# Kernel optimization log

Measured on AMD Instinct MI355X. Metric: run time of the kernel, lower is better.

Reference implementation:

```python
import jax, jax.numpy as jnp
import numpy as np

NUM_HEADS = 2
LN_EPS = 1e-5


def layer_norm(x, w, b):
    mu = jnp.mean(x, axis=-1, keepdims=True)
    var = jnp.mean(jnp.square(x - mu), axis=-1, keepdims=True)
    return (x - mu) * jax.lax.rsqrt(var + LN_EPS) * w + b


def setup_inputs() -> dict:
    key = jax.random.key(0)
    ks = jax.random.split(key, 8)
    B, N, C = 8, 2048, 1024
    H = 2 * C  # mlp hidden
    s = lambda fan_in: 1.0 / np.sqrt(fan_in)
    return {
        "x": jax.random.normal(ks[0], (B, N, C), dtype=jnp.float32),
        "ln1_w": jnp.ones((C,), jnp.float32),
        "ln1_b": jnp.zeros((C,), jnp.float32),
        "qkv_w": jax.random.normal(ks[1], (C, 3 * C), jnp.float32) * s(C),
        "qkv_b": jnp.zeros((3 * C,), jnp.float32),
        "proj_w": jax.random.normal(ks[2], (C, C), jnp.float32) * s(C),
        "proj_b": jnp.zeros((C,), jnp.float32),
        "ln2_w": jnp.ones((C,), jnp.float32),
        "ln2_b": jnp.zeros((C,), jnp.float32),
        "mlp_w1": jax.random.normal(ks[3], (C, H), jnp.float32) * s(C),
        "mlp_b1": jnp.zeros((H,), jnp.float32),
        "mlp_w2": jax.random.normal(ks[4], (H, C), jnp.float32) * s(H),
        "mlp_b2": jnp.zeros((C,), jnp.float32),
    }


def reference(x, ln1_w, ln1_b, qkv_w, qkv_b, proj_w, proj_b, ln2_w, ln2_b,
              mlp_w1, mlp_b1, mlp_w2, mlp_b2):
    B, N, C = x.shape
    h = NUM_HEADS
    d = C // h
    scale = d ** -0.5

    # --- attention branch ---
    xn = layer_norm(x, ln1_w, ln1_b)
    qkv = (xn @ qkv_w + qkv_b).reshape(B, N, 3, h, d)
    q, k, v = jnp.moveaxis(qkv, 2, 0)          # each [B, N, h, d]
    q = jnp.swapaxes(q, 1, 2)                  # [B, h, N, d]
    k = jnp.swapaxes(k, 1, 2)
    v = jnp.swapaxes(v, 1, 2)
    attn = jnp.einsum("bhnd,bhmd->bhnm", q, k) * scale
    attn = jax.nn.softmax(attn, axis=-1)       # [B, h, N, N]
    out = jnp.einsum("bhnm,bhmd->bhnd", attn, v)
    out = jnp.swapaxes(out, 1, 2).reshape(B, N, C)
    out = out @ proj_w + proj_b
    x = x + out

    # --- mlp branch ---
    xn = layer_norm(x, ln2_w, ln2_b)
    hdn = jax.nn.gelu(xn @ mlp_w1 + mlp_b1, approximate=False)
    x = x + (hdn @ mlp_w2 + mlp_b2)
    return x
```

## Files before the change

kernel.cpp:

```cpp
#include <hip/hip_runtime.h>
#include <hip/hip_bf16.h>
#include <math.h>

#define TILE 128
#define BK 32

using short8  = __attribute__((ext_vector_type(8))) short;
using short4v = __attribute__((ext_vector_type(4))) short;
using f32x4   = __attribute__((ext_vector_type(4))) float;
typedef __hip_bfloat16 bf16;

constexpr int BB = 8, SEQ = 2048, C = 1024, H3 = 3072, DH = 512, MH = 2048;
constexpr int MR = BB * SEQ;

enum {
  F_TRANSB = 1,
  F_GELU   = 2,
  F_RES    = 4,
  F_OUTBF16= 8,
  F_BIAS   = 16,
  F_SCALE  = 32,
  F_RESF32 = 64
};

struct ZOffs { long long a[16]; long long b[16]; long long c[16]; };

__device__ __forceinline__ float bf2f(bf16 h) { return __bfloat162float(h); }

__device__ __forceinline__ void gload16(const void* g, void* l) {
  __builtin_amdgcn_global_load_lds(
      (const __attribute__((address_space(1))) unsigned int*)g,
      (__attribute__((address_space(3))) unsigned int*)l, 16, 0, 0);
}

template<int FLAGS>
__global__ __launch_bounds__(256) void gemm_k(
    const bf16* __restrict__ A,
    const bf16* __restrict__ B,
    void* __restrict__ Dst,
    const float* __restrict__ bias,
    const void* __restrict__ res,
    int K, int lda, int ldb, int ldc,
    float scale, ZOffs zo)
{
  __shared__ __align__(16) unsigned short As[TILE * BK];
  __shared__ __align__(16) unsigned short Bs[TILE * BK];
  const int tid = threadIdx.x;
  const int z = blockIdx.z;
  const int m0 = blockIdx.y * TILE, n0 = blockIdx.x * TILE;
  const bf16* Ab = A + zo.a[z];
  const bf16* Bb = B + zo.b[z];
  const long long coff = zo.c[z];
  const int wave = tid >> 6, lane = tid & 63;
  const int wm = (wave & 1) << 6, wn = (wave >> 1) << 6;
  const int lr = lane & 15, lq = lane >> 4;

  int srow[2], skb[2];
  #pragma unroll
  for (int i = 0; i < 2; i++) {
    int c = tid + (i << 8);
    srow[i] = c >> 2;
    skb[i]  = (c & 3) ^ ((srow[i] >> 1) & 3);
  }
  const bf16* Asrc[2]; const bf16* Bsrc[2] = {nullptr, nullptr};
  #pragma unroll
  for (int i = 0; i < 2; i++)
    Asrc[i] = Ab + (size_t)(m0 + srow[i]) * lda + skb[i] * 8;
  if (FLAGS & F_TRANSB) {
    #pragma unroll
    for (int i = 0; i < 2; i++)
      Bsrc[i] = Bb + (size_t)(n0 + srow[i]) * ldb + skb[i] * 8;
  }

  f32x4 acc[4][4] = {};
  const int swl = (lr >> 1) & 3;

  for (int k0 = 0; k0 < K; k0 += BK) {
    #pragma unroll
    for (int i = 0; i < 2; i++)
      gload16(Asrc[i] + k0, &As[(tid + (i << 8)) * 8]);
    if (FLAGS & F_TRANSB) {
      #pragma unroll
      for (int i = 0; i < 2; i++)
        gload16(Bsrc[i] + k0, &Bs[(tid + (i << 8)) * 8]);
    } else {
      #pragma unroll
      for (int i = 0; i < 2; i++) {
        int c = tid + (i << 8);
        int kk = c >> 4, nn = (c & 15) << 3;
        unsigned short tmp[8];
        *(uint4*)tmp = *(const uint4*)(Bb + (size_t)(k0 + kk) * ldb + n0 + nn);
        #pragma unroll
        for (int j = 0; j < 8; j++) {
          int n = nn + j;
          Bs[n * BK + (((kk >> 3) ^ ((n >> 1) & 3)) << 3) + (kk & 7)] = tmp[j];
        }
      }
    }
    __syncthreads();
    short8 af[4], bfr[4];
    #pragma unroll
    for (int mi = 0; mi < 4; mi++)
      af[mi] = *(const short8*)&As[(wm + mi * 16 + lr) * BK + ((lq ^ swl) << 3)];
    #pragma unroll
    for (int ni = 0; ni < 4; ni++)
      bfr[ni] = *(const short8*)&Bs[(wn + ni * 16 + lr) * BK + ((lq ^ swl) << 3)];
    #pragma unroll
    for (int mi = 0; mi < 4; mi++)
      #pragma unroll
      for (int ni = 0; ni < 4; ni++)
        acc[mi][ni] = __builtin_amdgcn_mfma_f32_16x16x32_bf16(
            af[mi], bfr[ni], acc[mi][ni], 0, 0, 0);
    __syncthreads();
  }

  #pragma unroll
  for (int mi = 0; mi < 4; mi++) {
    #pragma unroll
    for (int ni = 0; ni < 4; ni++) {
      int col = n0 + wn + ni * 16 + lr;
      float bv = (FLAGS & F_BIAS) ? bias[col] : 0.0f;
      #pragma unroll
      for (int r = 0; r < 4; r++) {
        int row = m0 + wm + mi * 16 + lq * 4 + r;
        float v = acc[mi][ni][r];
        if (FLAGS & F_SCALE) v *= scale;
        v += bv;
        if (FLAGS & F_GELU) v = 0.5f * v * (1.0f + erff(v * 0.70710678118654752f));
        if (FLAGS & F_RES) {
          size_t ridx = (size_t)row * ldc + col;
          v += (FLAGS & F_RESF32) ? ((const float*)res)[ridx]
                                  : bf2f(((const bf16*)res)[ridx]);
        }
        size_t idx = (size_t)coff + (size_t)row * ldc + col;
        if (FLAGS & F_OUTBF16) ((bf16*)Dst)[idx] = __float2bfloat16(v);
        else                   ((float*)Dst)[idx] = v;
      }
    }
  }
}

template<int FLAGS>
__global__ __launch_bounds__(512, 2) void gemm256_k(
    const bf16* __restrict__ A,
    const bf16* __restrict__ B,
    void* __restrict__ Dst,
    const float* __restrict__ bias,
    const void* __restrict__ res,
    int K, int lda, int ldb, int ldc,
    float scale, ZOffs zo)
{
  static_assert(FLAGS & F_TRANSB, "gemm256_k requires B^T layout");
  extern __shared__ __align__(16) unsigned short smem[];

  const int tid = threadIdx.x;
  const int z = blockIdx.z;

  const int gx = gridDim.x;
  const int nwg = gx * gridDim.y;
  const int wg = blockIdx.y * gx + blockIdx.x;
  const int cpx = nwg >> 3;
  const int swz = (wg & 7) * cpx + (wg >> 3);
  const int m0 = (swz / gx) * 256, n0 = (swz % gx) * 256;

  const bf16* Ab = A + zo.a[z];
  const bf16* Bb = B + zo.b[z];
  const long long coff = zo.c[z];
  const int wave = tid >> 6, lane = tid & 63;
  const int wm = wave >> 2, wn = wave & 3;
  const int lr = lane & 15, lq = lane >> 4;
  const int swl = (lr >> 1) & 3;
  const int kcol = (lq ^ swl) << 3;

  const int c0 = tid, c1 = tid + 512;
  const int row0 = c0 >> 2, sl0 = (c0 & 3) ^ ((row0 >> 1) & 3);
  const int row1 = c1 >> 2, sl1 = (c1 & 3) ^ ((row1 >> 1) & 3);
  const bf16* sA0 = Ab + (size_t)(m0 + row0) * lda + sl0 * 8;
  const bf16* sA1 = Ab + (size_t)(m0 + row1) * lda + sl1 * 8;
  const bf16* sB0 = Bb + (size_t)(n0 + row0) * ldb + sl0 * 8;
  const bf16* sB1 = Bb + (size_t)(n0 + row1) * ldb + sl1 * 8;
  const int dst0 = c0 * 8, dst1 = c1 * 8;

  const int nt = K >> 5;

#define STAGE(ks_, D_)                                                         \
  do {                                                                         \
    gload16(sA0 + (ks_), (D_) + dst0);                                         \
    gload16(sA1 + (ks_), (D_) + dst1);                                         \
    gload16(sB0 + (ks_), (D_) + 8192 + dst0);                                  \
    gload16(sB1 + (ks_), (D_) + 8192 + dst1);                                  \
  } while (0)

  STAGE(0, smem);
  if (nt > 1) STAGE(32, smem + 16384);

  f32x4 acc[8][4] = {};
  short8 af[4], bf4[4];
  int bc = 0, bs = 2;

  for (int t = 0; t < nt; ++t) {
    if (t == nt - 1) asm volatile("s_waitcnt vmcnt(0)" ::: "memory");
    else             asm volatile("s_waitcnt vmcnt(4)" ::: "memory");
    __builtin_amdgcn_s_barrier();
    asm volatile("" ::: "memory");

    if (t + 2 < nt) STAGE((t + 2) * 32, smem + bs * 16384);

    const unsigned short* At = smem + bc * 16384;
    const unsigned short* Bt = At + 8192;

    #pragma unroll
    for (int n_ = 0; n_ < 4; ++n_)
      bf4[n_] = *(const short8*)&Bt[(wn * 64 + n_ * 16 + lr) * 32 + kcol];
    #pragma unroll
    for (int mh = 0; mh < 2; ++mh) {
      #pragma unroll
      for (int m_ = 0; m_ < 4; ++m_)
        af[m_] = *(const short8*)&At[(wm * 128 + mh * 64 + m_ * 16 + lr) * 32 + kcol];
      __builtin_amdgcn_s_setprio(1);
      #pragma unroll
      for (int m_ = 0; m_ < 4; ++m_)
        #pragma unroll
        for (int n_ = 0; n_ < 4; ++n_)
          acc[mh * 4 + m_][n_] = __builtin_amdgcn_mfma_f32_16x16x32_bf16(
              af[m_], bf4[n_], acc[mh * 4 + m_][n_], 0, 0, 0);
      __builtin_amdgcn_s_setprio(0);
    }
    bc = bc == 2 ? 0 : bc + 1;
    bs = bs == 2 ? 0 : bs + 1;
  }

#undef STAGE

  const int colBase = n0 + wn * 64 + lr;
  float bv[4];
  #pragma unroll
  for (int n = 0; n < 4; ++n)
    bv[n] = (FLAGS & F_BIAS) ? bias[colBase + n * 16] : 0.0f;
  #pragma unroll
  for (int m = 0; m < 8; ++m) {
    #pragma unroll
    for (int n = 0; n < 4; ++n) {
      const int col = colBase + n * 16;
      #pragma unroll
      for (int r = 0; r < 4; ++r) {
        const int row = m0 + wm * 128 + m * 16 + lq * 4 + r;
        float v = acc[m][n][r];
        if (FLAGS & F_SCALE) v *= scale;
        v += bv[n];
        if (FLAGS & F_GELU) v = 0.5f * v * (1.0f + erff(v * 0.70710678118654752f));
        if (FLAGS & F_RES) {
          size_t ridx = (size_t)row * ldc + col;
          v += (FLAGS & F_RESF32) ? ((const float*)res)[ridx]
                                  : bf2f(((const bf16*)res)[ridx]);
        }
        size_t idx = (size_t)coff + (size_t)row * ldc + col;
        if (FLAGS & F_OUTBF16) ((bf16*)Dst)[idx] = __float2bfloat16(v);
        else                   ((float*)Dst)[idx] = v;
      }
    }
  }
}

__global__ __launch_bounds__(256) void tconv_kernel(
    const float* __restrict__ src, bf16* __restrict__ dst, int K, int N)
{
  __shared__ float t[32][33];
  int n0 = blockIdx.x * 32, k0 = blockIdx.y * 32;
  int c = threadIdx.x & 31, r = threadIdx.x >> 5;
  #pragma unroll
  for (int i = 0; i < 4; i++)
    t[r + i * 8][c] = src[(size_t)(k0 + r + i * 8) * N + n0 + c];
  __syncthreads();
  #pragma unroll
  for (int i = 0; i < 4; i++)
    dst[(size_t)(n0 + r + i * 8) * K + k0 + c] = __float2bfloat16(t[c][r + i * 8]);
}

__global__ __launch_bounds__(256) void vtrans_kernel(
    const bf16* __restrict__ qkv, bf16* __restrict__ vt)
{
  __shared__ unsigned short t[32][33];
  int bh = blockIdx.z, b = bh >> 1, h = bh & 1;
  int n0 = blockIdx.x * 32, d0 = blockIdx.y * 32;
  int c = threadIdx.x & 31, r = threadIdx.x >> 5;
  const bf16* src = qkv + (size_t)b * SEQ * H3 + 2 * C + (size_t)h * DH;
  #pragma unroll
  for (int i = 0; i < 4; i++)
    t[r + i * 8][c] = *(const unsigned short*)&src[(size_t)(n0 + r + i * 8) * H3 + d0 + c];
  __syncthreads();
  bf16* dst = vt + ((size_t)bh * DH + d0) * SEQ + n0;
  #pragma unroll
  for (int i = 0; i < 4; i++)
    *(unsigned short*)&dst[(size_t)(r + i * 8) * SEQ + c] = t[c][r + i * 8];
}

__device__ __forceinline__ void ld4(const float* p, float v[4]) {
  const float4 t = *(const float4*)p;
  v[0] = t.x; v[1] = t.y; v[2] = t.z; v[3] = t.w;
}
__device__ __forceinline__ void ld4(const bf16* p, float v[4]) {
  short4v t = *(const short4v*)p;
  #pragma unroll
  for (int i = 0; i < 4; ++i) v[i] = bf2f(((const bf16*)&t)[i]);
}

template<typename T>
__global__ __launch_bounds__(256) void ln_kernel(
    const T* __restrict__ x,
    const float* __restrict__ w,
    const float* __restrict__ b,
    bf16* __restrict__ out)
{
  __shared__ float sm[4], sm2[4];
  int row = blockIdx.x, tid = threadIdx.x;
  float v[4];
  ld4(x + (size_t)row * 1024 + tid * 4, v);
  float s  = v[0] + v[1] + v[2] + v[3];
  float sq = v[0]*v[0] + v[1]*v[1] + v[2]*v[2] + v[3]*v[3];
  #pragma unroll
  for (int o = 32; o > 0; o >>= 1) {
    s  += __shfl_down(s, o, 64);
    sq += __shfl_down(sq, o, 64);
  }
  int wvi = tid >> 6, lnn = tid & 63;
  if (lnn == 0) { sm[wvi] = s; sm2[wvi] = sq; }
  __syncthreads();
  s  = sm[0] + sm[1] + sm[2] + sm[3];
  sq = sm2[0] + sm2[1] + sm2[2] + sm2[3];
  float mean = s * (1.0f / 1024.0f);
  float var  = sq * (1.0f / 1024.0f) - mean * mean;
  float rs = rsqrtf(var + 1e-5f);
  float wv4[4], bv4[4];
  ld4(w + tid * 4, wv4);
  ld4(b + tid * 4, bv4);
  short4v o4;
  #pragma unroll
  for (int i = 0; i < 4; ++i)
    ((bf16*)&o4)[i] = __float2bfloat16((v[i] - mean) * rs * wv4[i] + bv4[i]);
  *(short4v*)&out[(size_t)row * 1024 + tid * 4] = o4;
}

__global__ __launch_bounds__(256) void softmax_kernel(
    bf16* __restrict__ sc)
{
  __shared__ float sm[4];
  int tid = threadIdx.x;
  size_t base = ((size_t)blockIdx.y * 2048 + blockIdx.x) * 2048 + (size_t)tid * 8;
  short8 sv = *(const short8*)&sc[base];
  float v[8], m = -1e30f;
  #pragma unroll
  for (int i = 0; i < 8; i++) { v[i] = bf2f(((const bf16*)&sv)[i]); m = fmaxf(m, v[i]); }
  #pragma unroll
  for (int o = 32; o > 0; o >>= 1) m = fmaxf(m, __shfl_down(m, o, 64));
  int wvi = tid >> 6, lnn = tid & 63;
  if (lnn == 0) sm[wvi] = m;
  __syncthreads();
  m = fmaxf(fmaxf(sm[0], sm[1]), fmaxf(sm[2], sm[3]));
  __syncthreads();
  float s = 0.f;
  #pragma unroll
  for (int i = 0; i < 8; i++) { v[i] = __expf(v[i] - m); s += v[i]; }
  #pragma unroll
  for (int o = 32; o > 0; o >>= 1) s += __shfl_down(s, o, 64);
  if (lnn == 0) sm[wvi] = s;
  __syncthreads();
  s = sm[0] + sm[1] + sm[2] + sm[3];
  float inv = 1.0f / s;
  short8 ov;
  #pragma unroll
  for (int i = 0; i < 8; i++)
    ((bf16*)&ov)[i] = __float2bfloat16(v[i] * inv);
  *(short8*)&sc[base] = ov;
}

#define G256(FL, grid_, A_, B_, D_, bias_, res_, K_, lda_, ldb_, ldc_, sc_, zo_)      \
  do {                                                                                \
    (void)hipFuncSetAttribute(reinterpret_cast<const void*>(&gemm256_k<(FL)>),        \
                              hipFuncAttributeMaxDynamicSharedMemorySize, 98304);     \
    hipLaunchKernelGGL((gemm256_k<(FL)>), grid_, dim3(512), 98304, stream,            \
                       A_, B_, D_, bias_, res_, K_, lda_, ldb_, ldc_, sc_, zo_);      \
  } while (0)

extern "C" void kernel_launch(void* const* d_in, const int* in_sizes, int n_in,
                              void* d_out, int out_size, void* d_ws, size_t ws_size,
                              hipStream_t stream) {
  const float* x      = (const float*)d_in[0];
  const float* ln1_w  = (const float*)d_in[1];
  const float* ln1_b  = (const float*)d_in[2];
  const float* qkv_w  = (const float*)d_in[3];
  const float* qkv_b  = (const float*)d_in[4];
  const float* proj_w = (const float*)d_in[5];
  const float* proj_b = (const float*)d_in[6];
  const float* ln2_w  = (const float*)d_in[7];
  const float* ln2_b  = (const float*)d_in[8];
  const float* mlp_w1 = (const float*)d_in[9];
  const float* mlp_b1 = (const float*)d_in[10];
  const float* mlp_w2 = (const float*)d_in[11];
  const float* mlp_b2 = (const float*)d_in[12];
  float* out = (float*)d_out;

  char* ws = (char*)d_ws;
  const size_t MB = 1ull << 20;
  bf16* qkvT  = (bf16*)ws;
  bf16* projT = qkvT + 3 * 1024 * 1024;
  bf16* w1T   = qkvT + 4 * 1024 * 1024;
  bf16* w2T   = qkvT + 6 * 1024 * 1024;
  bf16* xn    = (bf16*)(ws + 16 * MB);
  bf16* qkvb  = (bf16*)(ws + 48 * MB);
  bf16* h1    = qkvb;
  bf16* Vt    = (bf16*)(ws + 144 * MB);

  int CH; bool useVt, x1f32;
  if      (ws_size >= 304 * MB) { CH = 16; useVt = true;  x1f32 = true;  }
  else if (ws_size >= 240 * MB) { CH = 8;  useVt = true;  x1f32 = true;  }
  else if (ws_size >= 208 * MB) { CH = 4;  useVt = true;  x1f32 = false; }
  else                          { CH = 4;  useVt = false; x1f32 = false; }
  char* R = ws + (useVt ? 176 * MB : 144 * MB);
  bf16*  scores = (bf16*)R;
  float* x1f    = (float*)R;
  bf16*  x1h    = (bf16*)R;

  ZOffs z0 = {};
  const float scale = 0.04419417382415922f;
  dim3 blk(256);

  hipLaunchKernelGGL(tconv_kernel, dim3(H3 / 32, C / 32), blk, 0, stream, qkv_w, qkvT, C, H3);
  hipLaunchKernelGGL(tconv_kernel, dim3(C / 32, C / 32), blk, 0, stream, proj_w, projT, C, C);
  hipLaunchKernelGGL(tconv_kernel, dim3(MH / 32, C / 32), blk, 0, stream, mlp_w1, w1T, C, MH);
  hipLaunchKernelGGL(tconv_kernel, dim3(C / 32, MH / 32), blk, 0, stream, mlp_w2, w2T, MH, C);

  hipLaunchKernelGGL((ln_kernel<float>), dim3(MR), blk, 0, stream, x, ln1_w, ln1_b, xn);

  G256(F_TRANSB | F_BIAS | F_OUTBF16, dim3(H3 / 256, MR / 256, 1),
       xn, qkvT, (void*)qkvb, qkv_b, nullptr, C, C, C, H3, 1.0f, z0);

  if (useVt)
    hipLaunchKernelGGL(vtrans_kernel, dim3(SEQ / 32, DH / 32, 16), blk, 0, stream, qkvb, Vt);

  for (int ch = 0; ch < 16 / CH; ch++) {
    ZOffs zq = {}, zp = {};
    for (int zz = 0; zz < CH; zz++) {
      int bh = ch * CH + zz, b = bh >> 1, hh = bh & 1;
      zq.a[zz] = (long long)b * SEQ * H3 + (long long)hh * DH;
      zq.b[zz] = (long long)b * SEQ * H3 + C + (long long)hh * DH;
      zq.c[zz] = (long long)zz * SEQ * SEQ;
      zp.a[zz] = (long long)zz * SEQ * SEQ;
      zp.b[zz] = useVt ? (long long)bh * DH * SEQ
                       : (long long)b * SEQ * H3 + 2 * C + (long long)hh * DH;
      zp.c[zz] = (long long)b * SEQ * C + (long long)hh * DH;
    }
    G256(F_TRANSB | F_SCALE | F_OUTBF16, dim3(SEQ / 256, SEQ / 256, CH),
         qkvb, qkvb, (void*)scores, nullptr, nullptr, DH, H3, H3, SEQ, scale, zq);
    hipLaunchKernelGGL(softmax_kernel, dim3(SEQ, CH), blk, 0, stream, scores);
    if (useVt)
      G256(F_TRANSB | F_OUTBF16, dim3(DH / 256, SEQ / 256, CH),
           scores, Vt, (void*)xn, nullptr, nullptr, SEQ, SEQ, SEQ, C, 1.0f, zp);
    else
      hipLaunchKernelGGL((gemm_k<F_OUTBF16>),
                         dim3(DH / TILE, SEQ / TILE, CH), blk, 0, stream,
                         scores, qkvb, (void*)xn, nullptr, nullptr, SEQ, SEQ, H3, C, 1.0f, zp);
  }

  if (x1f32) {
    G256(F_TRANSB | F_BIAS | F_RES | F_RESF32, dim3(C / 256, MR / 256, 1),
         xn, projT, (void*)x1f, proj_b, (const void*)x, C, C, C, C, 1.0f, z0);
    hipLaunchKernelGGL((ln_kernel<float>), dim3(MR), blk, 0, stream, x1f, ln2_w, ln2_b, xn);
  } else {
    G256(F_TRANSB | F_BIAS | F_RES | F_RESF32 | F_OUTBF16, dim3(C / 256, MR / 256, 1),
         xn, projT, (void*)x1h, proj_b, (const void*)x, C, C, C, C, 1.0f, z0);
    hipLaunchKernelGGL((ln_kernel<bf16>), dim3(MR), blk, 0, stream, x1h, ln2_w, ln2_b, xn);
  }

  G256(F_TRANSB | F_BIAS | F_GELU | F_OUTBF16, dim3(MH / 256, MR / 256, 1),
       xn, w1T, (void*)h1, mlp_b1, nullptr, C, C, C, MH, 1.0f, z0);

  if (x1f32) {
    G256(F_TRANSB | F_BIAS | F_RES | F_RESF32, dim3(C / 256, MR / 256, 1),
         h1, w2T, (void*)out, mlp_b2, (const void*)x1f, MH, MH, MH, C, 1.0f, z0);
  } else {
    G256(F_TRANSB | F_BIAS | F_RES, dim3(C / 256, MR / 256, 1),
         h1, w2T, (void*)out, mlp_b2, (const void*)x1h, MH, MH, MH, C, 1.0f, z0);
  }
}
```

Baseline: 801.9 us.

## Deepen GEMM pipeline to four LDS stages with register-prefetched fragments; fast GELU

The 256-tile GEMM moves from a three-stage to a four-stage LDS ring (128KB dynamic shared memory). The loop is unrolled by two so the next tile's A/B fragments are read into registers while the current MFMAs run, overlapping LDS reads with compute. GELU in the epilogue switches from erf to a tanh-form sigmoid approximation built on __expf, which cuts transcendental cost but adds a small numeric deviation. The larger LDS footprint may limit occupancy, and the unroll assumes an even tile count.

Result: faster. 782.2 us (-2.5%).

```diff
diff --git a/kernel.cpp b/kernel.cpp
--- a/kernel.cpp
+++ b/kernel.cpp
@@ -31,6 +31,12 @@
   __builtin_amdgcn_global_load_lds(
       (const __attribute__((address_space(1))) unsigned int*)g,
       (__attribute__((address_space(3))) unsigned int*)l, 16, 0, 0);
+}
+
+__device__ __forceinline__ float gelu_fast(float v) {
+  float u2 = v * (1.5957691216057308f + 0.0713548162726009f * v * v);
+  float e  = __expf(u2);
+  return v - v * (1.0f / (e + 1.0f));
 }
 
 template<int FLAGS>
@@ -126,7 +132,7 @@
         float v = acc[mi][ni][r];
         if (FLAGS & F_SCALE) v *= scale;
         v += bv;
-        if (FLAGS & F_GELU) v = 0.5f * v * (1.0f + erff(v * 0.70710678118654752f));
+        if (FLAGS & F_GELU) v = gelu_fast(v);
         if (FLAGS & F_RES) {
           size_t ridx = (size_t)row * ldc + col;
           v += (FLAGS & F_RESF32) ? ((const float*)res)[ridx]
@@ -191,46 +197,69 @@
     gload16(sB1 + (ks_), (D_) + 8192 + dst1);                                  \
   } while (0)
 
+#define RD_B(dst_, base_)                                                      \
+  _Pragma("unroll")                                                            \
+  for (int n_ = 0; n_ < 4; ++n_)                                               \
+    dst_[n_] = *(const short8*)&(base_)[8192 + (wn * 64 + n_ * 16 + lr) * 32 + kcol];
+#define RD_A0(dst_, base_)                                                     \
+  _Pragma("unroll")                                                            \
+  for (int m_ = 0; m_ < 4; ++m_)                                               \
+    dst_[m_] = *(const short8*)&(base_)[(wm * 128 + m_ * 16 + lr) * 32 + kcol];
+#define RD_A1(dst_, base_)                                                     \
+  _Pragma("unroll")                                                            \
+  for (int m_ = 0; m_ < 4; ++m_)                                               \
+    dst_[m_] = *(const short8*)&(base_)[(wm * 128 + 64 + m_ * 16 + lr) * 32 + kcol];
+#define MMH(mh_, A_, B_)                                                       \
+  __builtin_amdgcn_s_setprio(1);                                               \
+  _Pragma("unroll")                                                            \
+  for (int m_ = 0; m_ < 4; ++m_)                                               \
+    _Pragma("unroll")                                                          \
+    for (int n_ = 0; n_ < 4; ++n_)                                             \
+      acc[(mh_) * 4 + m_][n_] = __builtin_amdgcn_mfma_f32_16x16x32_bf16(       \
+          A_[m_], B_[n_], acc[(mh_) * 4 + m_][n_], 0, 0, 0);                   \
+  __builtin_amdgcn_s_setprio(0);
+
   STAGE(0, smem);
   if (nt > 1) STAGE(32, smem + 16384);
+  if (nt > 2) STAGE(64, smem + 32768);
+  if (nt > 2)      asm volatile("s_waitcnt vmcnt(8)" ::: "memory");
+  else if (nt > 1) asm volatile("s_waitcnt vmcnt(4)" ::: "memory");
+  else             asm volatile("s_waitcnt vmcnt(0)" ::: "memory");
+  __builtin_amdgcn_s_barrier();
+  asm volatile("" ::: "memory");
 
   f32x4 acc[8][4] = {};
-  short8 af[4], bf4[4];
-  int bc = 0, bs = 2;
-
-  for (int t = 0; t < nt; ++t) {
-    if (t == nt - 1) asm volatile("s_waitcnt vmcnt(0)" ::: "memory");
-    else             asm volatile("s_waitcnt vmcnt(4)" ::: "memory");
-    __builtin_amdgcn_s_barrier();
-    asm volatile("" ::: "memory");
-
-    if (t + 2 < nt) STAGE((t + 2) * 32, smem + bs * 16384);
-
-    const unsigned short* At = smem + bc * 16384;
-    const unsigned short* Bt = At + 8192;
-
-    #pragma unroll
-    for (int n_ = 0; n_ < 4; ++n_)
-      bf4[n_] = *(const short8*)&Bt[(wn * 64 + n_ * 16 + lr) * 32 + kcol];
-    #pragma unroll
-    for (int mh = 0; mh < 2; ++mh) {
-      #pragma unroll
-      for (int m_ = 0; m_ < 4; ++m_)
-        af[m_] = *(const short8*)&At[(wm * 128 + mh * 64 + m_ * 16 + lr) * 32 + kcol];
-      __builtin_amdgcn_s_setprio(1);
-      #pragma unroll
-      for (int m_ = 0; m_ < 4; ++m_)
-        #pragma unroll
-        for (int n_ = 0; n_ < 4; ++n_)
-          acc[mh * 4 + m_][n_] = __builtin_amdgcn_mfma_f32_16x16x32_bf16(
-              af[m_], bf4[n_], acc[mh * 4 + m_][n_], 0, 0, 0);
-      __builtin_amdgcn_s_setprio(0);
-    }
-    bc = bc == 2 ? 0 : bc + 1;
-    bs = bs == 2 ? 0 : bs + 1;
+  short8 afA[4], afB[4], af1[4], bfA[4], bfB[4];
+  RD_B(bfA, smem);
+  RD_A0(afA, smem);
+
+#define HALF(t_, AFC, BFC, AFN, BFN)                                           \
+  do {                                                                         \
+    if ((t_) >= nt - 2) asm volatile("s_waitcnt vmcnt(0)" ::: "memory");       \
+    else                asm volatile("s_waitcnt vmcnt(4)" ::: "memory");       \
+    __builtin_amdgcn_s_barrier();                                              \
+    asm volatile("" ::: "memory");                                             \
+    if ((t_) + 3 < nt) STAGE(((t_) + 3) * 32, smem + (((t_) + 3) & 3) * 16384);\
+    const unsigned short* At_ = smem + ((t_) & 3) * 16384;                     \
+    const unsigned short* An_ = smem + (((t_) + 1) & 3) * 16384;               \
+    RD_A1(af1, At_);                                                           \
+    __builtin_amdgcn_sched_barrier(0);                                         \
+    MMH(0, AFC, BFC);                                                          \
+    if ((t_) + 1 < nt) { RD_B(BFN, An_); RD_A0(AFN, An_); }                    \
+    MMH(1, af1, BFC);                                                          \
+  } while (0)
+
+  for (int t = 0; t < nt; t += 2) {
+    HALF(t, afA, bfA, afB, bfB);
+    HALF(t + 1, afB, bfB, afA, bfA);
   }
 
 #undef STAGE
+#undef RD_B
+#undef RD_A0
+#undef RD_A1
+#undef MMH
+#undef HALF
 
   const int colBase = n0 + wn * 64 + lr;
   float bv[4];
@@ -248,7 +277,7 @@
         float v = acc[m][n][r];
         if (FLAGS & F_SCALE) v *= scale;
         v += bv[n];
-        if (FLAGS & F_GELU) v = 0.5f * v * (1.0f + erff(v * 0.70710678118654752f));
+        if (FLAGS & F_GELU) v = gelu_fast(v);
         if (FLAGS & F_RES) {
           size_t ridx = (size_t)row * ldc + col;
           v += (FLAGS & F_RESF32) ? ((const float*)res)[ridx]
@@ -377,8 +406,8 @@
 #define G256(FL, grid_, A_, B_, D_, bias_, res_, K_, lda_, ldb_, ldc_, sc_, zo_)      \
   do {                                                                                \
     (void)hipFuncSetAttribute(reinterpret_cast<const void*>(&gemm256_k<(FL)>),        \
-                              hipFuncAttributeMaxDynamicSharedMemorySize, 98304);     \
-    hipLaunchKernelGGL((gemm256_k<(FL)>), grid_, dim3(512), 98304, stream,            \
+                              hipFuncAttributeMaxDynamicSharedMemorySize, 131072);    \
+    hipLaunchKernelGGL((gemm256_k<(FL)>), grid_, dim3(512), 131072, stream,           \
                        A_, B_, D_, bias_, res_, K_, lda_, ldb_, ldc_, sc_, zo_);      \
   } while (0)
 
```
